# Optimization experiments

Hardware: AMD Instinct MI355X
Metric: run time of the kernel (lower is better)

The kernel has to match this reference:

```python
import jax, jax.numpy as jnp
import numpy as np

D_MODEL = 768
N_HEADS = 12
D_KEYS = 64
D_LLM = 4096
D_INNER = N_HEADS * D_KEYS  # 768


def setup_inputs() -> dict:
    key = jax.random.key(0)
    ks = jax.random.split(key, 12)
    inp = {
        "target_embedding": jax.random.normal(ks[0], (8, 1024, D_MODEL), dtype=jnp.float32),
        "source_embedding": jax.random.normal(ks[1], (1000, D_LLM), dtype=jnp.float32),
        "value_embedding": jax.random.normal(ks[2], (1000, D_LLM), dtype=jnp.float32),
        # Linear params stored as [in, out] (y = x @ W + b)
        "Wq": jax.random.normal(ks[3], (D_MODEL, D_INNER), dtype=jnp.float32) * 0.02,
        "bq": jnp.zeros((D_INNER,), dtype=jnp.float32),
        "Wk": jax.random.normal(ks[4], (D_LLM, D_INNER), dtype=jnp.float32) * 0.02,
        "bk": jnp.zeros((D_INNER,), dtype=jnp.float32),
        "Wv": jax.random.normal(ks[5], (D_LLM, D_INNER), dtype=jnp.float32) * 0.02,
        "bv": jnp.zeros((D_INNER,), dtype=jnp.float32),
        "Wo": jax.random.normal(ks[6], (D_INNER, D_LLM), dtype=jnp.float32) * 0.02,
        "bo": jnp.zeros((D_LLM,), dtype=jnp.float32),
    }
    return inp


def reference(target_embedding, source_embedding, value_embedding,
              Wq, bq, Wk, bk, Wv, bv, Wo, bo):
    B, L, _ = target_embedding.shape
    S, _ = source_embedding.shape
    H, E = N_HEADS, D_KEYS
    # projections
    q = (target_embedding @ Wq + bq).reshape(B, L, H, E)  # [B,L,H,E]
    k = (source_embedding @ Wk + bk).reshape(S, H, E)     # [S,H,E] broadcast over batch
    v = (value_embedding @ Wv + bv).reshape(S, H, E)      # [S,H,E]
    scale = 1.0 / np.sqrt(E).astype(np.float32)
    scores = jnp.einsum('blhe,she->bhls', q, k) * scale   # [B,H,L,S]
    A = jax.nn.softmax(scores, axis=-1)                   # dropout is identity at eval
    out = jnp.einsum('bhls,she->blhe', A, v).reshape(B, L, H * E)
    return out @ Wo + bo                                  # [B,L,d_llm]
```

## Files before the change

kernel.cpp:

```cpp
#include <hip/hip_runtime.h>
#include <cstdint>
#include <type_traits>


typedef unsigned short u16;
typedef __attribute__((ext_vector_type(8))) short bf16x8;
typedef __attribute__((ext_vector_type(4))) float f32x4;
typedef __attribute__((ext_vector_type(16))) float f32x16;
typedef __attribute__((ext_vector_type(4))) float fvec4;
typedef __attribute__((ext_vector_type(4))) unsigned short u16x4;
typedef __attribute__((ext_vector_type(4))) unsigned int u32x4;
typedef __attribute__((ext_vector_type(2))) unsigned int u32x2;

using gld_src_t = const __attribute__((address_space(1))) void*;
using gld_dst_t = __attribute__((address_space(3))) void*;

static __device__ __forceinline__ u16 bf16_rne(float f) {
  uint32_t u = __builtin_bit_cast(uint32_t, f);
  u += 0x7fffu + ((u >> 16) & 1u);
  return (u16)(u >> 16);
}

static __device__ __forceinline__ float exp2_fast(float x) {
  float r; asm("v_exp_f32 %0, %1" : "=v"(r) : "v"(x)); return r;
}

static __device__ __forceinline__ uint32_t pk_bf16(float a, float b) {
  return (uint32_t)bf16_rne(a) | ((uint32_t)bf16_rne(b) << 16);
}

__global__ void convert_pad_bf16(const float* __restrict__ in, u16* __restrict__ out,
                                 int validR, int C, long n4) {
  long stride = (long)gridDim.x * blockDim.x;
  for (long i = (long)blockIdx.x * blockDim.x + threadIdx.x; i < n4; i += stride) {
    long e = i << 2;
    int r = (int)(e / C);
    u16x4 o;
    if (r < validR) {
      fvec4 v = *(const fvec4*)(in + e);
      o[0] = bf16_rne(v[0]); o[1] = bf16_rne(v[1]);
      o[2] = bf16_rne(v[2]); o[3] = bf16_rne(v[3]);
    } else {
      o[0] = 0; o[1] = 0; o[2] = 0; o[3] = 0;
    }
    *(u16x4*)(out + e) = o;
  }
}

template <bool F32IN>
__global__ void transpose_to_bf16(const void* __restrict__ inv, u16* __restrict__ out,
                                  int R, int C) {
  __shared__ u16 tile[32][33];
  int bc = blockIdx.x * 32, br = blockIdx.y * 32;
  int tx = threadIdx.x & 31, ty = threadIdx.x >> 5;
#pragma unroll
  for (int i = 0; i < 4; ++i) {
    int r = br + ty + i * 8, c = bc + tx;
    u16 bits = 0;
    if (r < R && c < C) {
      if constexpr (F32IN) bits = bf16_rne(((const float*)inv)[(size_t)r * C + c]);
      else                 bits = ((const u16*)inv)[(size_t)r * C + c];
    }
    tile[ty + i * 8][tx] = bits;
  }
  __syncthreads();
#pragma unroll
  for (int i = 0; i < 4; ++i) {
    int orow = bc + ty + i * 8, oc = br + tx;
    if (orow < C && oc < R) out[(size_t)orow * R + oc] = tile[tx][ty + i * 8];
  }
}

template <typename CT>
__global__ __launch_bounds__(256, 2) void gemm_bt_128p(
    const u16* __restrict__ A, const u16* __restrict__ B,
    const float* __restrict__ bias, CT* __restrict__ C,
    int N, int K, float escale) {
  __shared__ u16 As[2][128 * 64];
  __shared__ u16 Bs[2][128 * 64];

  const int tid = threadIdx.x, lane = tid & 63, w = tid >> 6;
  const int lr = lane & 15, lg = lane >> 4;
  const int wr = (w >> 1) * 64, wc = (w & 1) * 64;

  const int nbx = N >> 7;
  const int bid = blockIdx.y * gridDim.x + blockIdx.x;
  const int cpx = (gridDim.x * gridDim.y) >> 3;
  const int swz = (bid & 7) * cpx + (bid >> 3);
  const int bm = (swz / nbx) * 128, bn = (swz % nbx) * 128;

  f32x4 acc[4][4] = {};

  auto STAGE = [&](int t, int buf) {
#pragma unroll
    for (int it = 0; it < 4; ++it) {
      const int s = it * 256 + tid;
      const int r = s >> 3;
      const int cg = (s & 7) ^ (r & 7);
      const int ldsb = (it * 256 + w * 64) * 16;
      __builtin_amdgcn_global_load_lds(
          (gld_src_t)(const void*)(A + (size_t)(bm + r) * K + t * 64 + cg * 8),
          (gld_dst_t)((char*)&As[buf][0] + ldsb), 16, 0, 0);
      __builtin_amdgcn_global_load_lds(
          (gld_src_t)(const void*)(B + (size_t)(bn + r) * K + t * 64 + cg * 8),
          (gld_dst_t)((char*)&Bs[buf][0] + ldsb), 16, 0, 0);
    }
  };

  auto LDF = [&](const u16* base, int R, int CB) {
    return *(const bf16x8*)((const char*)base + (size_t)R * 128 + (CB ^ ((R & 7) << 4)));
  };

  STAGE(0, 0);

  const int nk = K >> 6;
  for (int t = 0; t < nk; ++t) {
    const int cur = t & 1;
    if (t + 1 < nk) {
      STAGE(t + 1, cur ^ 1);
      asm volatile("s_waitcnt vmcnt(8)" ::: "memory");
    } else {
      asm volatile("s_waitcnt vmcnt(0)" ::: "memory");
    }
    __builtin_amdgcn_s_barrier();
    __builtin_amdgcn_sched_barrier(0);

    const u16* as = &As[cur][0];
    const u16* bs = &Bs[cur][0];

    bf16x8 af[4][2], bfr[4][2];
#pragma unroll
    for (int m = 0; m < 4; ++m)
#pragma unroll
      for (int kk = 0; kk < 2; ++kk)
        af[m][kk] = LDF(as, wr + m * 16 + lr, kk * 64 + lg * 16);
#pragma unroll
    for (int n = 0; n < 4; ++n)
#pragma unroll
      for (int kk = 0; kk < 2; ++kk)
        bfr[n][kk] = LDF(bs, wc + n * 16 + lr, kk * 64 + lg * 16);

    __builtin_amdgcn_s_setprio(1);
#pragma unroll
    for (int kk = 0; kk < 2; ++kk)
#pragma unroll
      for (int m = 0; m < 4; ++m)
#pragma unroll
        for (int n = 0; n < 4; ++n)
          acc[m][n] = __builtin_amdgcn_mfma_f32_16x16x32_bf16(
              af[m][kk], bfr[n][kk], acc[m][n], 0, 0, 0);
    __builtin_amdgcn_s_setprio(0);

    __builtin_amdgcn_sched_barrier(0);
    __builtin_amdgcn_s_barrier();
  }

#pragma unroll
  for (int n = 0; n < 4; ++n) {
    const int col = bn + wc + n * 16 + lr;
    const float bv = bias[col];
#pragma unroll
    for (int m = 0; m < 4; ++m) {
      const int row0 = bm + wr + m * 16 + lg * 4;
#pragma unroll
      for (int r = 0; r < 4; ++r) {
        float v = (acc[m][n][r] + bv) * escale;
        if constexpr (std::is_same<CT, u16>::value)
          C[(size_t)(row0 + r) * N + col] = bf16_rne(v);
        else
          C[(size_t)(row0 + r) * N + col] = v;
      }
    }
  }
}

__global__ __launch_bounds__(512, 2) void gemm_bt_256p(
    const u16* __restrict__ A, const u16* __restrict__ B,
    const float* __restrict__ bias, float* __restrict__ C,
    int N, int K) {
  __shared__ u16 As[4][128 * 64];
  __shared__ u16 Bs[4][128 * 64];

  const int tid = threadIdx.x, lane = tid & 63, w = tid >> 6;
  const int lr = lane & 15, lg = lane >> 4;
  const int wr = w >> 2, wcol = w & 3;

  const int nbx = N >> 8;
  const int bid = blockIdx.y * gridDim.x + blockIdx.x;
  const int cpx = (gridDim.x * gridDim.y) >> 3;
  const int swz = (bid & 7) * cpx + (bid >> 3);
  const int bm = (swz / nbx) * 256, bn = (swz % nbx) * 256;

  f32x4 acc[8][4] = {};

  auto STAGE_UNIT = [&](int t, int buf, int mat) {
#pragma unroll
    for (int it = 0; it < 2; ++it) {
      const int s = it * 512 + tid;
      const int rp = s >> 3;
      const int cl = (s & 7) ^ (rp & 7);
      const int gr = (cl >> 2) * 128 + rp;
      const int gc = cl & 3;
      const int ldsb = (it * 512 + w * 64) * 16;
      const u16* src = (mat ? B : A) + (size_t)((mat ? bn : bm) + gr) * K + t * 32 + gc * 8;
      __builtin_amdgcn_global_load_lds((gld_src_t)(const void*)src,
          (gld_dst_t)((char*)(mat ? &Bs[buf][0] : &As[buf][0]) + ldsb), 16, 0, 0);
    }
  };

  auto LDF = [&](const u16* base, int gr, int klg) {
    const int byte = (gr & 127) * 128 + (((((gr >> 7) * 4 + klg) << 4)) ^ ((gr & 7) << 4));
    return *(const bf16x8*)((const char*)base + byte);
  };

  STAGE_UNIT(0, 0, 0); STAGE_UNIT(0, 0, 1);
  STAGE_UNIT(1, 1, 0); STAGE_UNIT(1, 1, 1);
  asm volatile("s_waitcnt vmcnt(4)" ::: "memory");
  __builtin_amdgcn_s_barrier();
  __builtin_amdgcn_sched_barrier(0);

  const int nk = K >> 5;
  bf16x8 bfr[4];
  for (int t = 0; t < nk; ++t) {
    const int cur = t & 3;
    const u16* as = &As[cur][0];
    const u16* bs = &Bs[cur][0];
#pragma unroll
    for (int p = 0; p < 2; ++p) {
      bf16x8 af[4];
#pragma unroll
      for (int m = 0; m < 4; ++m)
        af[m] = LDF(as, wr * 128 + (p * 4 + m) * 16 + lr, lg);
      if (p == 0) {
#pragma unroll
        for (int n = 0; n < 4; ++n)
          bfr[n] = LDF(bs, wcol * 64 + n * 16 + lr, lg);
      }
      if (t + 2 < nk) STAGE_UNIT(t + 2, (t + 2) & 3, p);
      if (p == 1) {
        if (t + 2 < nk)      asm volatile("s_waitcnt vmcnt(4)" ::: "memory");
        else if (t + 1 < nk) asm volatile("s_waitcnt vmcnt(0)" ::: "memory");
      }
      __builtin_amdgcn_s_barrier();
      __builtin_amdgcn_sched_barrier(0);
      __builtin_amdgcn_s_setprio(1);
#pragma unroll
      for (int m = 0; m < 4; ++m)
#pragma unroll
        for (int n = 0; n < 4; ++n)
          acc[p * 4 + m][n] = __builtin_amdgcn_mfma_f32_16x16x32_bf16(
              af[m], bfr[n], acc[p * 4 + m][n], 0, 0, 0);
      __builtin_amdgcn_s_setprio(0);
      __builtin_amdgcn_sched_barrier(0);
    }
  }

  float bv[4];
#pragma unroll
  for (int nf = 0; nf < 4; ++nf) bv[nf] = bias[bn + wcol * 64 + nf * 16 + lr];
#pragma unroll
  for (int mf = 0; mf < 8; ++mf) {
    const int row0 = bm + wr * 128 + mf * 16 + lg * 4;
#pragma unroll
    for (int nf = 0; nf < 4; ++nf) {
      const int col = bn + wcol * 64 + nf * 16 + lr;
#pragma unroll
      for (int r = 0; r < 4; ++r)
        C[(size_t)(row0 + r) * N + col] = acc[mf][nf][r] + bv[nf];
    }
  }
}

__global__ __launch_bounds__(256) void gemm_kv_splitk(
    const u16* __restrict__ Sb, const u16* __restrict__ Vbi,
    const u16* __restrict__ WkT, const u16* __restrict__ WvT,
    float* __restrict__ part) {
  const int z = blockIdx.z;
  const u16* A = (z >> 2) ? Vbi : Sb;
  const u16* B = (z >> 2) ? WvT : WkT;
  float* C = part + (size_t)z * (1024 * 768);
  const int kofs = (z & 3) * 1024;

  __shared__ u16 As[128 * 32];
  __shared__ u16 Bs[128 * 32];
  const int tid = threadIdx.x, w = tid >> 6, lane = tid & 63;
  const int lr = lane & 15, lg = lane >> 4;
  const int bm = blockIdx.y * 128, bn = blockIdx.x * 128;
  const int wr = (w >> 1) * 64, wc = (w & 1) * 64;
  f32x4 acc[4][4] = {};

  for (int kt = 0; kt < 32; ++kt) {
#pragma unroll
    for (int j = 0; j < 2; ++j) {
      int cb = j * 256 + w * 64;
      int c = cb + lane;
      const u16* gA = A + (size_t)(bm + (c >> 2)) * 4096 + kofs + kt * 32 + (c & 3) * 8;
      __builtin_amdgcn_global_load_lds((gld_src_t)(const void*)gA,
                                       (gld_dst_t)(As + (size_t)cb * 8), 16, 0, 0);
      const u16* gB = B + (size_t)(bn + (c >> 2)) * 4096 + kofs + kt * 32 + (c & 3) * 8;
      __builtin_amdgcn_global_load_lds((gld_src_t)(const void*)gB,
                                       (gld_dst_t)(Bs + (size_t)cb * 8), 16, 0, 0);
    }
    __syncthreads();
    bf16x8 af[4], bfr[4];
#pragma unroll
    for (int m = 0; m < 4; ++m)
      af[m] = *(const bf16x8*)(As + (wr + m * 16 + lr) * 32 + lg * 8);
#pragma unroll
    for (int n = 0; n < 4; ++n)
      bfr[n] = *(const bf16x8*)(Bs + (wc + n * 16 + lr) * 32 + lg * 8);
#pragma unroll
    for (int m = 0; m < 4; ++m)
#pragma unroll
      for (int n = 0; n < 4; ++n)
        acc[m][n] = __builtin_amdgcn_mfma_f32_16x16x32_bf16(af[m], bfr[n], acc[m][n], 0, 0, 0);
    __syncthreads();
  }
#pragma unroll
  for (int n = 0; n < 4; ++n) {
    int col = bn + wc + n * 16 + lr;
#pragma unroll
    for (int m = 0; m < 4; ++m) {
      int row0 = bm + wr + m * 16 + lg * 4;
#pragma unroll
      for (int r = 0; r < 4; ++r)
        C[(size_t)(row0 + r) * 768 + col] = acc[m][n][r];
    }
  }
}

__global__ __launch_bounds__(256) void kv_reduce(const float* __restrict__ part,
                                                 const float* __restrict__ bk,
                                                 const float* __restrict__ bv,
                                                 u16* __restrict__ Kp, u16* __restrict__ Vp) {
  const int mat = blockIdx.y;
  const long e = ((long)blockIdx.x * 256 + threadIdx.x) * 4;
  const float* p0 = part + (size_t)mat * 4 * 786432 + e;
  fvec4 s = *(const fvec4*)p0;
  s += *(const fvec4*)(p0 + 786432);
  s += *(const fvec4*)(p0 + 2 * 786432);
  s += *(const fvec4*)(p0 + 3 * 786432);
  const float* bias = mat ? bv : bk;
  int col = (int)(e % 768);
  fvec4 bb = *(const fvec4*)(bias + col);
  s += bb;
  u16x4 o;
  o[0] = bf16_rne(s[0]); o[1] = bf16_rne(s[1]); o[2] = bf16_rne(s[2]); o[3] = bf16_rne(s[3]);
  u16* dst = mat ? Vp : Kp;
  *(u16x4*)(dst + e) = o;
}

__global__ __launch_bounds__(256, 3) void attn_flash(
    const u16* __restrict__ Q,
    const u16* __restrict__ Kb,
    const u16* __restrict__ VT,
    u16* __restrict__ O) {
  constexpr int DM = 768, SPAD = 1024;
  __shared__ u16 Ks[2][64 * 64];
  __shared__ u16 VTs[2][64 * 64];

  const int tid = threadIdx.x, w = tid >> 6, lane = tid & 63;
  const int q5 = lane & 31, hi = lane >> 5, l7 = lane & 7;
  const int h = blockIdx.y;
  const int qrow = blockIdx.x * 128 + w * 32 + q5;

  bf16x8 qf[4];
#pragma unroll
  for (int dstep = 0; dstep < 4; ++dstep)
    qf[dstep] = *(const bf16x8*)(Q + (size_t)qrow * DM + h * 64 + dstep * 16 + hi * 8);

  auto STAGE = [&](int ch, int buf) {
#pragma unroll
    for (int it = 0; it < 2; ++it) {
      int slot = it * 256 + w * 64 + lane;
      int row = slot >> 3;
      int cg = (slot & 7) ^ (row & 7);
      __builtin_amdgcn_global_load_lds(
          (gld_src_t)(const void*)(Kb + (size_t)(ch * 64 + row) * DM + h * 64 + cg * 8),
          (gld_dst_t)(&Ks[buf][(size_t)(it * 256 + w * 64) * 8]), 16, 0, 0);
      __builtin_amdgcn_global_load_lds(
          (gld_src_t)(const void*)(VT + (size_t)(h * 64 + row) * SPAD + ch * 64 + cg * 8),
          (gld_dst_t)(&VTs[buf][(size_t)(it * 256 + w * 64) * 8]), 16, 0, 0);
    }
  };

  STAGE(0, 0);

  float m_run = -3.0e38f, l_part = 0.0f;
  f32x16 oa0 = {}, oa1 = {};

  for (int ch = 0; ch < 16; ++ch) {
    const int cur = ch & 1;
    if (ch < 15) {
      STAGE(ch + 1, cur ^ 1);
      asm volatile("s_waitcnt vmcnt(4)" ::: "memory");
    } else {
      asm volatile("s_waitcnt vmcnt(0)" ::: "memory");
    }
    __builtin_amdgcn_s_barrier();
    __builtin_amdgcn_sched_barrier(0);

    const char* kbase = (const char*)&Ks[cur][0];
    const char* vbase = (const char*)&VTs[cur][0];

    f32x16 sc0 = {}, sc1 = {};
#pragma unroll
    for (int dstep = 0; dstep < 4; ++dstep) {
      const int colb = (dstep * 32 + hi * 16);
      bf16x8 kf0 = *(const bf16x8*)(kbase + (size_t)q5 * 128 + (colb ^ (l7 << 4)));
      bf16x8 kf1 = *(const bf16x8*)(kbase + (size_t)(32 + q5) * 128 + (colb ^ (l7 << 4)));
      sc0 = __builtin_amdgcn_mfma_f32_32x32x16_bf16(kf0, qf[dstep], sc0, 0, 0, 0);
      sc1 = __builtin_amdgcn_mfma_f32_32x32x16_bf16(kf1, qf[dstep], sc1, 0, 0, 0);
    }
    if (ch == 15) {
#pragma unroll
      for (int r = 4; r < 16; ++r) sc1[r] = -3.0e38f;
    }

    float mi = sc0[0];
#pragma unroll
    for (int r = 1; r < 16; ++r) mi = fmaxf(mi, sc0[r]);
#pragma unroll
    for (int r = 0; r < 16; ++r) mi = fmaxf(mi, sc1[r]);
    float cm = fmaxf(mi, __shfl_xor(mi, 32, 64));

    if (__any(cm > m_run + 8.0f)) {
      float mn = fmaxf(m_run, cm);
      float fsc = exp2_fast(m_run - mn);
      m_run = mn;
      l_part *= fsc;
#pragma unroll
      for (int r = 0; r < 16; ++r) { oa0[r] *= fsc; oa1[r] *= fsc; }
    }

#pragma unroll
    for (int r = 0; r < 16; ++r) {
      float p0 = exp2_fast(sc0[r] - m_run); l_part += p0; sc0[r] = p0;
      float p1 = exp2_fast(sc1[r] - m_run); l_part += p1; sc1[r] = p1;
    }

#pragma unroll
    for (int st = 0; st < 2; ++st) {
#pragma unroll
      for (int ks = 0; ks < 2; ++ks) {
        float pv0, pv1, pv2, pv3, pv4, pv5, pv6, pv7;
        if (st == 0) {
          if (ks == 0) { pv0=sc0[0];pv1=sc0[1];pv2=sc0[2];pv3=sc0[3];pv4=sc0[4];pv5=sc0[5];pv6=sc0[6];pv7=sc0[7]; }
          else         { pv0=sc0[8];pv1=sc0[9];pv2=sc0[10];pv3=sc0[11];pv4=sc0[12];pv5=sc0[13];pv6=sc0[14];pv7=sc0[15]; }
        } else {
          if (ks == 0) { pv0=sc1[0];pv1=sc1[1];pv2=sc1[2];pv3=sc1[3];pv4=sc1[4];pv5=sc1[5];pv6=sc1[6];pv7=sc1[7]; }
          else         { pv0=sc1[8];pv1=sc1[9];pv2=sc1[10];pv3=sc1[11];pv4=sc1[12];pv5=sc1[13];pv6=sc1[14];pv7=sc1[15]; }
        }
        uint32_t a = pk_bf16(pv0, pv1), b = pk_bf16(pv2, pv3);
        uint32_t c = pk_bf16(pv4, pv5), d = pk_bf16(pv6, pv7);
        uint32_t sa = (uint32_t)__shfl_xor((int)a, 32, 64);
        uint32_t sb = (uint32_t)__shfl_xor((int)b, 32, 64);
        uint32_t sc_ = (uint32_t)__shfl_xor((int)c, 32, 64);
        uint32_t sd = (uint32_t)__shfl_xor((int)d, 32, 64);
        u32x4 jw;
        jw[0] = hi ? sc_ : a;
        jw[1] = hi ? sd  : b;
        jw[2] = hi ? c   : sa;
        jw[3] = hi ? d   : sb;
        bf16x8 pB = __builtin_bit_cast(bf16x8, jw);
        const int colb = (st * 64 + ks * 32 + hi * 16);
#pragma unroll
        for (int dt = 0; dt < 2; ++dt) {
          bf16x8 vtf = *(const bf16x8*)(vbase + (size_t)(dt * 32 + q5) * 128 + (colb ^ (l7 << 4)));
          if (dt == 0) oa0 = __builtin_amdgcn_mfma_f32_32x32x16_bf16(vtf, pB, oa0, 0, 0, 0);
          else         oa1 = __builtin_amdgcn_mfma_f32_32x32x16_bf16(vtf, pB, oa1, 0, 0, 0);
        }
      }
    }
    __builtin_amdgcn_sched_barrier(0);
    __builtin_amdgcn_s_barrier();
  }

  float ool = 1.0f / (l_part + __shfl_xor(l_part, 32, 64));
  u16* obase = O + (size_t)qrow * DM + h * 64;
#pragma unroll
  for (int dt = 0; dt < 2; ++dt) {
#pragma unroll
    for (int g = 0; g < 4; ++g) {
      float v0, v1, v2, v3;
      if (dt == 0) { v0 = oa0[4*g]; v1 = oa0[4*g+1]; v2 = oa0[4*g+2]; v3 = oa0[4*g+3]; }
      else         { v0 = oa1[4*g]; v1 = oa1[4*g+1]; v2 = oa1[4*g+2]; v3 = oa1[4*g+3]; }
      u32x2 st2;
      st2[0] = pk_bf16(v0 * ool, v1 * ool);
      st2[1] = pk_bf16(v2 * ool, v3 * ool);
      *(u32x2*)(obase + dt * 32 + g * 8 + hi * 4) = st2;
    }
  }
}

extern "C" void kernel_launch(void* const* d_in, const int* in_sizes, int n_in,
                              void* d_out, int out_size, void* d_ws, size_t ws_size,
                              hipStream_t stream) {
  (void)in_sizes; (void)n_in; (void)out_size; (void)ws_size;
  const float* target = (const float*)d_in[0];
  const float* source = (const float*)d_in[1];
  const float* value  = (const float*)d_in[2];
  const float* Wq = (const float*)d_in[3];
  const float* bq = (const float*)d_in[4];
  const float* Wk = (const float*)d_in[5];
  const float* bk = (const float*)d_in[6];
  const float* Wv = (const float*)d_in[7];
  const float* bv = (const float*)d_in[8];
  const float* Wo = (const float*)d_in[9];
  const float* bo = (const float*)d_in[10];
  float* out = (float*)d_out;

  char* ws = (char*)d_ws;
  size_t off = 0;
  auto carve = [&](size_t bytes) { void* p = ws + off; off += (bytes + 255) & ~(size_t)255; return p; };
  u16* Xb  = (u16*)carve(8192ull * 768 * 2);
  u16* Sb  = (u16*)carve(1024ull * 4096 * 2);
  u16* Vbi = (u16*)carve(1024ull * 4096 * 2);
  u16* WqT = (u16*)carve(768ull * 768 * 2);
  u16* WkT = (u16*)carve(768ull * 4096 * 2);
  u16* WvT = (u16*)carve(768ull * 4096 * 2);
  u16* WoT = (u16*)carve(4096ull * 768 * 2);
  u16* Qb  = (u16*)carve(8192ull * 768 * 2);
  u16* Kp  = (u16*)carve(1024ull * 768 * 2);
  u16* Vp  = (u16*)carve(1024ull * 768 * 2);
  u16* VTp = (u16*)carve(768ull * 1024 * 2);
  u16* Ob  = (u16*)carve(8192ull * 768 * 2);

  const float SCL = 0.18033688011112042f;

  convert_pad_bf16<<<2048, 256, 0, stream>>>(target, Xb, 8192, 768, (8192ll * 768) / 4);
  convert_pad_bf16<<<2048, 256, 0, stream>>>(source, Sb, 1000, 4096, (1024ll * 4096) / 4);
  convert_pad_bf16<<<2048, 256, 0, stream>>>(value,  Vbi, 1000, 4096, (1024ll * 4096) / 4);
  transpose_to_bf16<true><<<dim3(24, 24),  256, 0, stream>>>(Wq, WqT, 768, 768);
  transpose_to_bf16<true><<<dim3(24, 128), 256, 0, stream>>>(Wk, WkT, 4096, 768);
  transpose_to_bf16<true><<<dim3(24, 128), 256, 0, stream>>>(Wv, WvT, 4096, 768);
  transpose_to_bf16<true><<<dim3(128, 24), 256, 0, stream>>>(Wo, WoT, 768, 4096);

  gemm_kv_splitk<<<dim3(6, 8, 8), 256, 0, stream>>>(Sb, Vbi, WkT, WvT, out);
  kv_reduce<<<dim3(768, 2), 256, 0, stream>>>(out, bk, bv, Kp, Vp);
  transpose_to_bf16<false><<<dim3(24, 32), 256, 0, stream>>>(Vp, VTp, 1024, 768);

  gemm_bt_128p<u16><<<dim3(6, 64), 256, 0, stream>>>(Xb, WqT, bq, Qb, 768, 768, SCL);

  attn_flash<<<dim3(64, 12), 256, 0, stream>>>(Qb, Kp, VTp, Ob);

  gemm_bt_256p<<<dim3(16, 32), 512, 0, stream>>>(Ob, WoT, bo, out, 4096, 768);
}
```

Measured before the change: 215.9 us.

## Software-pipeline flash attention with triple-buffered LDS and hardware bf16 packing

Restructures the attention loop so the QK^T MFMAs for the next key chunk are issued before the softmax and PV work of the current chunk. LDS K/V staging moves from double to triple buffering to keep prefetch two chunks ahead. It also swaps the manual bf16 round-and-pack for the v_cvt_pk_bf16_f32 instruction. The cost is more registers for a second score tile and more LDS per block, which may lower occupancy under launch_bounds(256,3).

Measured after the change: 220.5 us. +2.1%, slower.

```diff
diff --git a/kernel.cpp b/kernel.cpp
--- a/kernel.cpp
+++ b/kernel.cpp
@@ -27,6 +27,12 @@
 
 static __device__ __forceinline__ uint32_t pk_bf16(float a, float b) {
   return (uint32_t)bf16_rne(a) | ((uint32_t)bf16_rne(b) << 16);
+}
+
+static __device__ __forceinline__ uint32_t cvtpk_bf16(float lo, float hi) {
+  uint32_t r;
+  asm("v_cvt_pk_bf16_f32 %0, %1, %2" : "=v"(r) : "v"(lo), "v"(hi));
+  return r;
 }
 
 __global__ void convert_pad_bf16(const float* __restrict__ in, u16* __restrict__ out,
@@ -356,8 +362,8 @@
     const u16* __restrict__ VT,
     u16* __restrict__ O) {
   constexpr int DM = 768, SPAD = 1024;
-  __shared__ u16 Ks[2][64 * 64];
-  __shared__ u16 VTs[2][64 * 64];
+  __shared__ u16 Ks[3][64 * 64];
+  __shared__ u16 VTs[3][64 * 64];
 
   const int tid = threadIdx.x, w = tid >> 6, lane = tid & 63;
   const int q5 = lane & 31, hi = lane >> 5, l7 = lane & 7;
@@ -384,46 +390,34 @@
     }
   };
 
-  STAGE(0, 0);
-
   float m_run = -3.0e38f, l_part = 0.0f;
   f32x16 oa0 = {}, oa1 = {};
 
-  for (int ch = 0; ch < 16; ++ch) {
-    const int cur = ch & 1;
-    if (ch < 15) {
-      STAGE(ch + 1, cur ^ 1);
-      asm volatile("s_waitcnt vmcnt(4)" ::: "memory");
-    } else {
-      asm volatile("s_waitcnt vmcnt(0)" ::: "memory");
-    }
-    __builtin_amdgcn_s_barrier();
-    __builtin_amdgcn_sched_barrier(0);
-
-    const char* kbase = (const char*)&Ks[cur][0];
-    const char* vbase = (const char*)&VTs[cur][0];
-
-    f32x16 sc0 = {}, sc1 = {};
+  auto QKT = [&](int cc, int buf, f32x16& s0, f32x16& s1) {
+    const char* kbase = (const char*)&Ks[buf][0];
+    s0 = f32x16{}; s1 = f32x16{};
 #pragma unroll
     for (int dstep = 0; dstep < 4; ++dstep) {
       const int colb = (dstep * 32 + hi * 16);
       bf16x8 kf0 = *(const bf16x8*)(kbase + (size_t)q5 * 128 + (colb ^ (l7 << 4)));
       bf16x8 kf1 = *(const bf16x8*)(kbase + (size_t)(32 + q5) * 128 + (colb ^ (l7 << 4)));
-      sc0 = __builtin_amdgcn_mfma_f32_32x32x16_bf16(kf0, qf[dstep], sc0, 0, 0, 0);
-      sc1 = __builtin_amdgcn_mfma_f32_32x32x16_bf16(kf1, qf[dstep], sc1, 0, 0, 0);
-    }
-    if (ch == 15) {
-#pragma unroll
-      for (int r = 4; r < 16; ++r) sc1[r] = -3.0e38f;
-    }
-
-    float mi = sc0[0];
-#pragma unroll
-    for (int r = 1; r < 16; ++r) mi = fmaxf(mi, sc0[r]);
-#pragma unroll
-    for (int r = 0; r < 16; ++r) mi = fmaxf(mi, sc1[r]);
+      s0 = __builtin_amdgcn_mfma_f32_32x32x16_bf16(kf0, qf[dstep], s0, 0, 0, 0);
+      s1 = __builtin_amdgcn_mfma_f32_32x32x16_bf16(kf1, qf[dstep], s1, 0, 0, 0);
+    }
+    if (cc == 15) {
+#pragma unroll
+      for (int r = 4; r < 16; ++r) s1[r] = -3.0e38f;
+    }
+  };
+
+  auto SMPV = [&](int buf, f32x16& s0, f32x16& s1) {
+    const char* vbase = (const char*)&VTs[buf][0];
+    float mi = s0[0];
+#pragma unroll
+    for (int r = 1; r < 16; ++r) mi = fmaxf(mi, s0[r]);
+#pragma unroll
+    for (int r = 0; r < 16; ++r) mi = fmaxf(mi, s1[r]);
     float cm = fmaxf(mi, __shfl_xor(mi, 32, 64));
-
     if (__any(cm > m_run + 8.0f)) {
       float mn = fmaxf(m_run, cm);
       float fsc = exp2_fast(m_run - mn);
@@ -432,27 +426,25 @@
 #pragma unroll
       for (int r = 0; r < 16; ++r) { oa0[r] *= fsc; oa1[r] *= fsc; }
     }
-
 #pragma unroll
     for (int r = 0; r < 16; ++r) {
-      float p0 = exp2_fast(sc0[r] - m_run); l_part += p0; sc0[r] = p0;
-      float p1 = exp2_fast(sc1[r] - m_run); l_part += p1; sc1[r] = p1;
-    }
-
+      float p0 = exp2_fast(s0[r] - m_run); l_part += p0; s0[r] = p0;
+      float p1 = exp2_fast(s1[r] - m_run); l_part += p1; s1[r] = p1;
+    }
 #pragma unroll
     for (int st = 0; st < 2; ++st) {
 #pragma unroll
       for (int ks = 0; ks < 2; ++ks) {
         float pv0, pv1, pv2, pv3, pv4, pv5, pv6, pv7;
         if (st == 0) {
-          if (ks == 0) { pv0=sc0[0];pv1=sc0[1];pv2=sc0[2];pv3=sc0[3];pv4=sc0[4];pv5=sc0[5];pv6=sc0[6];pv7=sc0[7]; }
-          else         { pv0=sc0[8];pv1=sc0[9];pv2=sc0[10];pv3=sc0[11];pv4=sc0[12];pv5=sc0[13];pv6=sc0[14];pv7=sc0[15]; }
+          if (ks == 0) { pv0=s0[0];pv1=s0[1];pv2=s0[2];pv3=s0[3];pv4=s0[4];pv5=s0[5];pv6=s0[6];pv7=s0[7]; }
+          else         { pv0=s0[8];pv1=s0[9];pv2=s0[10];pv3=s0[11];pv4=s0[12];pv5=s0[13];pv6=s0[14];pv7=s0[15]; }
         } else {
-          if (ks == 0) { pv0=sc1[0];pv1=sc1[1];pv2=sc1[2];pv3=sc1[3];pv4=sc1[4];pv5=sc1[5];pv6=sc1[6];pv7=sc1[7]; }
-          else         { pv0=sc1[8];pv1=sc1[9];pv2=sc1[10];pv3=sc1[11];pv4=sc1[12];pv5=sc1[13];pv6=sc1[14];pv7=sc1[15]; }
+          if (ks == 0) { pv0=s1[0];pv1=s1[1];pv2=s1[2];pv3=s1[3];pv4=s1[4];pv5=s1[5];pv6=s1[6];pv7=s1[7]; }
+          else         { pv0=s1[8];pv1=s1[9];pv2=s1[10];pv3=s1[11];pv4=s1[12];pv5=s1[13];pv6=s1[14];pv7=s1[15]; }
         }
-        uint32_t a = pk_bf16(pv0, pv1), b = pk_bf16(pv2, pv3);
-        uint32_t c = pk_bf16(pv4, pv5), d = pk_bf16(pv6, pv7);
+        uint32_t a = cvtpk_bf16(pv0, pv1), b = cvtpk_bf16(pv2, pv3);
+        uint32_t c = cvtpk_bf16(pv4, pv5), d = cvtpk_bf16(pv6, pv7);
         uint32_t sa = (uint32_t)__shfl_xor((int)a, 32, 64);
         uint32_t sb = (uint32_t)__shfl_xor((int)b, 32, 64);
         uint32_t sc_ = (uint32_t)__shfl_xor((int)c, 32, 64);
@@ -472,8 +464,41 @@
         }
       }
     }
-    __builtin_amdgcn_sched_barrier(0);
+  };
+
+  STAGE(0, 0);
+  STAGE(1, 1);
+  f32x16 sA0, sA1, sB0, sB1;
+  asm volatile("s_waitcnt vmcnt(4)" ::: "memory");
+  __builtin_amdgcn_s_barrier();
+  __builtin_amdgcn_sched_barrier(0);
+  QKT(0, 0, sA0, sA1);
+
+  for (int c = 0; c < 16; c += 2) {
+    if (c + 2 < 16) STAGE(c + 2, (c + 2) % 3);
+    if (c + 1 < 16) {
+      if (c + 2 < 16) asm volatile("s_waitcnt vmcnt(4)" ::: "memory");
+      else            asm volatile("s_waitcnt vmcnt(0)" ::: "memory");
+      __builtin_amdgcn_s_barrier();
+      __builtin_amdgcn_sched_barrier(0);
+      QKT(c + 1, (c + 1) % 3, sB0, sB1);
+    }
+    SMPV(c % 3, sA0, sA1);
     __builtin_amdgcn_s_barrier();
+
+    const int c1 = c + 1;
+    if (c1 < 16) {
+      if (c1 + 2 < 16) STAGE(c1 + 2, (c1 + 2) % 3);
+      if (c1 + 1 < 16) {
+        if (c1 + 2 < 16) asm volatile("s_waitcnt vmcnt(4)" ::: "memory");
+        else             asm volatile("s_waitcnt vmcnt(0)" ::: "memory");
+        __builtin_amdgcn_s_barrier();
+        __builtin_amdgcn_sched_barrier(0);
+        QKT(c1 + 1, (c1 + 1) % 3, sA0, sA1);
+      }
+      SMPV(c1 % 3, sB0, sB1);
+      __builtin_amdgcn_s_barrier();
+    }
   }
 
   float ool = 1.0f / (l_part + __shfl_xor(l_part, 32, 64));
@@ -486,8 +511,8 @@
       if (dt == 0) { v0 = oa0[4*g]; v1 = oa0[4*g+1]; v2 = oa0[4*g+2]; v3 = oa0[4*g+3]; }
       else         { v0 = oa1[4*g]; v1 = oa1[4*g+1]; v2 = oa1[4*g+2]; v3 = oa1[4*g+3]; }
       u32x2 st2;
-      st2[0] = pk_bf16(v0 * ool, v1 * ool);
-      st2[1] = pk_bf16(v2 * ool, v3 * ool);
+      st2[0] = cvtpk_bf16(v0 * ool, v1 * ool);
+      st2[1] = cvtpk_bf16(v2 * ool, v3 * ool);
       *(u32x2*)(obase + dt * 32 + g * 8 + hi * 4) = st2;
     }
   }
```
